# Optimization experiments

Measured on AMD Instinct MI355X. Metric: run time of the kernel, lower is better.

Reference implementation:

```python
import jax, jax.numpy as jnp
import numpy as np

N = 50000      # nodes
E = 800000     # edges
IN = 128       # input feature dim
HID = 64       # out_channels per head
HEADS = 2
OUT = 40       # num classes
SLOPE = 0.2    # leaky relu negative slope
EPS = 1e-16    # PyG softmax denominator epsilon


def _xavier(key, shape):
    fan_out, fan_in = shape[0], shape[1]
    a = float(np.sqrt(6.0 / (fan_in + fan_out)))
    return jax.random.uniform(key, shape, minval=-a, maxval=a, dtype=jnp.float32)


def setup_inputs() -> dict:
    key = jax.random.key(0)
    ks = jax.random.split(key, 16)
    x = jax.random.normal(ks[0], (N, IN), dtype=jnp.float32)
    edge_index = jax.random.randint(ks[1], (2, E), 0, N, dtype=jnp.int64)
    # GAT layer 1: lin_l == lin_r (shared), weight [H*C, in], att [C, H]
    W1 = _xavier(ks[2], (HEADS * HID, IN))
    b1 = jnp.zeros((HEADS * HID,), jnp.float32)
    al1 = _xavier(ks[3], (HID, HEADS))
    ar1 = _xavier(ks[4], (HID, HEADS))
    # GAT layer 2: input dim = heads*hidden
    W2 = _xavier(ks[5], (HEADS * HID, HEADS * HID))
    b2 = jnp.zeros((HEADS * HID,), jnp.float32)
    al2 = _xavier(ks[6], (HID, HEADS))
    ar2 = _xavier(ks[7], (HID, HEADS))
    # post_mp: Linear(heads*hid, hid) -> Linear(hid, out)
    Wp1 = _xavier(ks[8], (HID, HEADS * HID))
    bp1 = jnp.zeros((HID,), jnp.float32)
    Wp2 = _xavier(ks[9], (OUT, HID))
    bp2 = jnp.zeros((OUT,), jnp.float32)
    return dict(x=x, edge_index=edge_index, W1=W1, b1=b1, al1=al1, ar1=ar1,
                W2=W2, b2=b2, al2=al2, ar2=ar2, Wp1=Wp1, bp1=bp1, Wp2=Wp2, bp2=bp2)


def gat_layer(x, edge_index, W, b, att_l, att_r):
    """One GAT layer: shared linear, per-edge leaky-relu scores,
    segment-softmax keyed by destination node, scatter-sum."""
    n = x.shape[0]
    xt = (x @ W.T + b).reshape(n, HEADS, HID)          # [N, H, C] (x_l == x_r)
    alpha_l = jnp.einsum('nhc,ch->nh', xt, att_l)      # [N, H]
    alpha_r = jnp.einsum('nhc,ch->nh', xt, att_r)      # [N, H]
    src, dst = edge_index[0], edge_index[1]            # j = source, i = dest
    e = jax.nn.leaky_relu(alpha_r[dst] + alpha_l[src], SLOPE)   # [E, H]
    # segment softmax over edges grouped by destination node
    seg_max = jax.ops.segment_max(e, dst, num_segments=n)       # [N, H]
    ex = jnp.exp(e - seg_max[dst])
    denom = jax.ops.segment_sum(ex, dst, num_segments=n)        # [N, H]
    alpha = ex / (denom[dst] + EPS)                              # [E, H]
    msg = alpha[:, :, None] * xt[src]                            # [E, H, C]
    out = jax.ops.segment_sum(msg, dst, num_segments=n)          # [N, H, C]
    return out.reshape(n, HEADS * HID)


def reference(x, edge_index, W1, b1, al1, ar1, W2, b2, al2, ar2, Wp1, bp1, Wp2, bp2):
    h = jax.nn.relu(gat_layer(x, edge_index, W1, b1, al1, ar1))
    h = jax.nn.relu(gat_layer(h, edge_index, W2, b2, al2, ar2))
    h = h @ Wp1.T + bp1
    h = h @ Wp2.T + bp2
    return jax.nn.log_softmax(h, axis=1)
```

## Files before the change

kernel.cpp:

```cpp
#include <hip/hip_runtime.h>
#include <hip/hip_fp16.h>
#include <cmath>

#define N_NODES 50000
#define N_EDGES 800000
#define F 128
#define OUT_DIM 40
#define SLOPE 0.2f
#define EPS_DEN 1e-16f

#define BK_SHIFT 7
#define BKSZ 128
#define NBK ((N_NODES + BKSZ - 1) / BKSZ)
#define BK_CAP2 2560
#define SC_CHUNK 2500
#define SC_BLOCKS ((N_EDGES + SC_CHUNK - 1) / SC_CHUNK)
#define GEMM_TILES ((N_NODES + 127) / 128)
#define A_BLOCKS (SC_BLOCKS + 25 + GEMM_TILES)
#define SMEM_BYTES 21504
#define POISON ((int)0xAAAAAAAA)

typedef _Float16 half8 __attribute__((ext_vector_type(8)));
typedef float floatx4 __attribute__((ext_vector_type(4)));

struct ScatterS { int sd[SC_CHUNK]; short sb[SC_CHUNK]; int h[NBK]; int lofs[NBK]; };
struct GemmS    { __half Ah[128][40]; __half Bh[128][40]; };
static_assert(sizeof(ScatterS) <= SMEM_BYTES, "scatter LDS");
static_assert(sizeof(GemmS)    <= SMEM_BYTES, "gemm LDS");

__device__ inline float4 load4(const float* p) { return *(const float4*)p; }
__device__ inline float4 load4(const __half* p) {
  uint2 u = *(const uint2*)p;
  float2 a = __half22float2(*(__half2*)&u.x);
  float2 b = __half22float2(*(__half2*)&u.y);
  return make_float4(a.x, a.y, b.x, b.y);
}

__device__ __forceinline__ void scatter_phase(const int* __restrict__ ei,
    int* __restrict__ bcur, int* __restrict__ pairs, int it, int tid, char* smem_) {
  ScatterS* S = (ScatterS*)smem_;
  for (int i = tid; i < NBK; i += 256) S->h[i] = 0;
  __syncthreads();
  int base = it * SC_CHUNK;
  int end = base + SC_CHUNK; if (end > N_EDGES) end = N_EDGES;
  int cnt = end - base;
  for (int e = base + tid; e < end; e += 256) {
    int s = ei[e];
    int d = ei[N_EDGES + e];
    int b = d >> BK_SHIFT;
    S->sd[e - base] = (s << BK_SHIFT) | (d & (BKSZ - 1));
    S->sb[e - base] = (short)b;
    atomicAdd(&S->h[b], 1);
  }
  __syncthreads();
  for (int i = tid; i < NBK; i += 256)
    if (S->h[i]) {
      S->lofs[i] = i * BK_CAP2 + (atomicAdd(&bcur[i], S->h[i]) - POISON);
      S->h[i] = 0;
    }
  __syncthreads();
  for (int i = tid; i < cnt; i += 256) {
    int b = S->sb[i];
    int pos = S->lofs[b] + atomicAdd(&S->h[b], 1);
    pairs[pos] = S->sd[i];
  }
}

__device__ __forceinline__ void combine_phase(const float* __restrict__ Wp1,
    const float* __restrict__ bp1, const float* __restrict__ Wp2,
    const float* __restrict__ bp2, __half* __restrict__ Wch,
    float* __restrict__ bc, int it, int tid) {
  if (it < 24) {
    int idx = it * 256 + tid;
    int o = idx >> 7, k = idx & 127;
    float s = 0.f;
    if (o < OUT_DIM) {
#pragma unroll 8
      for (int j = 0; j < 64; ++j) s += Wp2[o * 64 + j] * Wp1[j * 128 + k];
    }
    Wch[o * 128 + k] = __float2half(s);
  } else if (tid < 48) {
    int o = tid;
    if (o < OUT_DIM) {
      float s = bp2[o];
      for (int j = 0; j < 64; ++j) s += Wp2[o * 64 + j] * bp1[j];
      bc[o] = s;
    } else {
      bc[o] = -1e30f;
    }
  }
}

template <typename T>
__device__ __forceinline__ void gemm_phase(const T* __restrict__ A,
    const float* __restrict__ W, const float* __restrict__ b,
    const float* __restrict__ attl, const float* __restrict__ attr,
    __half* __restrict__ Ch, float* __restrict__ al, float* __restrict__ ar,
    int nrows, int tile, int tid, char* smem_) {
  GemmS* S = (GemmS*)smem_;
  int lane = tid & 63, wid = tid >> 6;
  int quad = lane >> 4, col = lane & 15;
  int r0 = tile * 128;
  int rowhalf = wid >> 1, colhalf = wid & 1;
  floatx4 acc[4][4] = {};
  for (int kc = 0; kc < 128; kc += 32) {
    for (int i = tid; i < 512; i += 256) {
      int row = i >> 2, seg = i & 3;
      int gr = r0 + row;
      float4 v0, v1;
      if (gr < nrows) {
        const T* p = A + (size_t)gr * 128 + kc + seg * 8;
        v0 = load4(p); v1 = load4(p + 4);
      } else { v0 = make_float4(0.f,0.f,0.f,0.f); v1 = v0; }
      __half2 h0 = __floats2half2_rn(v0.x, v0.y), h1 = __floats2half2_rn(v0.z, v0.w);
      __half2 h2 = __floats2half2_rn(v1.x, v1.y), h3 = __floats2half2_rn(v1.z, v1.w);
      uint4 pk; pk.x = *(unsigned*)&h0; pk.y = *(unsigned*)&h1;
      pk.z = *(unsigned*)&h2; pk.w = *(unsigned*)&h3;
      *(uint4*)&S->Ah[row][seg * 8] = pk;
      const float* q = W + (size_t)row * 128 + kc + seg * 8;
      float4 w0 = *(const float4*)q, w1 = *(const float4*)(q + 4);
      __half2 g0 = __floats2half2_rn(w0.x, w0.y), g1 = __floats2half2_rn(w0.z, w0.w);
      __half2 g2 = __floats2half2_rn(w1.x, w1.y), g3 = __floats2half2_rn(w1.z, w1.w);
      uint4 qk; qk.x = *(unsigned*)&g0; qk.y = *(unsigned*)&g1;
      qk.z = *(unsigned*)&g2; qk.w = *(unsigned*)&g3;
      *(uint4*)&S->Bh[row][seg * 8] = qk;
    }
    __syncthreads();
    half8 afr[4], bfr[4];
#pragma unroll
    for (int rt = 0; rt < 4; ++rt)
      afr[rt] = *(const half8*)&S->Ah[rowhalf * 64 + rt * 16 + col][quad * 8];
#pragma unroll
    for (int ct = 0; ct < 4; ++ct)
      bfr[ct] = *(const half8*)&S->Bh[colhalf * 64 + ct * 16 + col][quad * 8];
#pragma unroll
    for (int rt = 0; rt < 4; ++rt)
#pragma unroll
      for (int ct = 0; ct < 4; ++ct)
        acc[rt][ct] = __builtin_amdgcn_mfma_f32_16x16x32_f16(afr[rt], bfr[ct],
                                                             acc[rt][ct], 0, 0, 0);
    __syncthreads();
  }
  int head = colhalf;
  float bj[4], wl4[4], wr4[4];
#pragma unroll
  for (int ct = 0; ct < 4; ++ct) {
    int c = ct * 16 + col;
    bj[ct] = b[head * 64 + c];
    wl4[ct] = attl[c * 2 + head];
    wr4[ct] = attr[c * 2 + head];
  }
#pragma unroll
  for (int rt = 0; rt < 4; ++rt) {
#pragma unroll
    for (int reg = 0; reg < 4; ++reg) {
      int gr = r0 + rowhalf * 64 + rt * 16 + quad * 4 + reg;
      bool ok = gr < nrows;
      float pl = 0.f, pr = 0.f;
#pragma unroll
      for (int ct = 0; ct < 4; ++ct) {
        float v = acc[rt][ct][reg] + bj[ct];
        pl += v * wl4[ct]; pr += v * wr4[ct];
        if (ok) Ch[(size_t)gr * F + head * 64 + ct * 16 + col] = __float2half(v);
      }
      pl += __shfl_xor(pl, 1, 64); pr += __shfl_xor(pr, 1, 64);
      pl += __shfl_xor(pl, 2, 64); pr += __shfl_xor(pr, 2, 64);
      pl += __shfl_xor(pl, 4, 64); pr += __shfl_xor(pr, 4, 64);
      pl += __shfl_xor(pl, 8, 64); pr += __shfl_xor(pr, 8, 64);
      if (ok && col == 0) { al[gr * 2 + head] = pl; ar[gr * 2 + head] = pr; }
    }
  }
}

__global__ __launch_bounds__(256) void kernelA(const int* __restrict__ ei,
    int* __restrict__ bcur, int* __restrict__ pairs,
    const float* __restrict__ Wp1, const float* __restrict__ bp1,
    const float* __restrict__ Wp2, const float* __restrict__ bp2,
    __half* __restrict__ Wch, float* __restrict__ bc,
    const float* __restrict__ x, const float* __restrict__ W1,
    const float* __restrict__ b1, const float* __restrict__ al1,
    const float* __restrict__ ar1, __half* __restrict__ xh,
    float* __restrict__ al, float* __restrict__ ar) {
  __shared__ __align__(16) char smem[SMEM_BYTES];
  int bid = blockIdx.x, tid = threadIdx.x;
  if (bid < SC_BLOCKS) {
    scatter_phase(ei, bcur, pairs, bid, tid, smem);
  } else if (bid < SC_BLOCKS + 25) {
    combine_phase(Wp1, bp1, Wp2, bp2, Wch, bc, bid - SC_BLOCKS, tid);
  } else {
    gemm_phase<float>(x, W1, b1, al1, ar1, xh, al, ar, N_NODES,
                      bid - SC_BLOCKS - 25, tid, smem);
  }
}

__global__ __launch_bounds__(256) void gemm2_kernel(const __half* __restrict__ hb,
    const float* __restrict__ W2, const float* __restrict__ b2,
    const float* __restrict__ al2, const float* __restrict__ ar2,
    __half* __restrict__ xh, float* __restrict__ al, float* __restrict__ ar) {
  __shared__ __align__(16) char smem[SMEM_BYTES];
  gemm_phase<__half>(hb, W2, b2, al2, ar2, xh, al, ar, N_NODES,
                     blockIdx.x, threadIdx.x, smem);
}

__global__ __launch_bounds__(256) void local_sort(const int* __restrict__ bcur,
    const int* __restrict__ pairs, int* __restrict__ rowstart,
    int* __restrict__ rowend, int* __restrict__ srcs) {
  __shared__ int buf[BK_CAP2];
  __shared__ int sorted[BK_CAP2];
  __shared__ int hist[BKSZ];
  __shared__ int cur[BKSZ];
  int tid = threadIdx.x;
  int b = blockIdx.x;
  int base = b * BK_CAP2;
  int cnt = bcur[b] - POISON;
  if (cnt > BK_CAP2) cnt = BK_CAP2;
  if (cnt < 0) cnt = 0;
  if (tid < BKSZ) hist[tid] = 0;
  __syncthreads();
  for (int i = tid; i < cnt; i += 256) {
    int p = pairs[base + i];
    buf[i] = p;
    atomicAdd(&hist[p & (BKSZ - 1)], 1);
  }
  __syncthreads();
  if (tid < 64) {
    int lane = tid;
    int carry = 0;
#pragma unroll
    for (int c = 0; c < BKSZ; c += 64) {
      int v = hist[c + lane];
      int x = v;
#pragma unroll
      for (int off = 1; off < 64; off <<= 1) {
        int t = __shfl_up(x, off, 64);
        if (lane >= off) x += t;
      }
      int excl = carry + x - v;
      cur[c + lane] = excl;
      int node = b * BKSZ + c + lane;
      if (node < N_NODES) {
        rowstart[node] = base + excl;
        rowend[node]   = base + excl + v;
      }
      carry += __shfl(x, 63, 64);
    }
  }
  __syncthreads();
  for (int i = tid; i < cnt; i += 256) {
    int p = buf[i];
    int pos = atomicAdd(&cur[p & (BKSZ - 1)], 1);
    sorted[pos] = p >> BK_SHIFT;
  }
  __syncthreads();
  for (int i = tid; i < cnt; i += 256)
    srcs[base + i] = sorted[i];
}

__global__ __launch_bounds__(256) void aggregate_kernel(const int* __restrict__ rowstart,
    const int* __restrict__ rowend, const int* __restrict__ srcs,
    const float* __restrict__ al, const float* __restrict__ ar,
    const __half* __restrict__ xh, __half* __restrict__ out, int n) {
  __shared__ float ebuf[4][2][64];
  __shared__ int   sbuf[4][64];
  int tid = threadIdx.x;
  int wid = tid >> 6, lane = tid & 63;
  int g = lane >> 4, q = lane & 15;
  int head = q >> 3;
  int node = blockIdx.x * 4 + wid;
  if (node >= n) return;
  int start = rowstart[node], end = rowend[node];
  float2 arv = *(const float2*)(ar + (size_t)node * 2);
  float ar0 = arv.x, ar1 = arv.y;
  const float* wrow = &ebuf[wid][head][0];
  const __half* xbase = xh + q * 8;
  float acc[8] = {};
  float dl0 = 0.f, dl1 = 0.f;
  for (int c = start; c < end; c += 64) {
    int j = c + lane;
    float e0 = 0.f, e1 = 0.f; int soff = 0;
    if (j < end) {
      int s = srcs[j];
      soff = s << BK_SHIFT;
      float2 a = *(const float2*)(al + (size_t)s * 2);
      float s0 = a.x + ar0; s0 = (s0 > 0.f) ? s0 : SLOPE * s0;
      float s1 = a.y + ar1; s1 = (s1 > 0.f) ? s1 : SLOPE * s1;
      e0 = __expf(s0); e1 = __expf(s1);
    }
    dl0 += e0; dl1 += e1;
    ebuf[wid][0][lane] = e0; ebuf[wid][1][lane] = e1; sbuf[wid][lane] = soff;
    __builtin_amdgcn_wave_barrier();
    int cend = end - c; if (cend > 64) cend = 64;
#pragma unroll 4
    for (int t = 0; t < cend; t += 4) {
      int te = t + g;
      if (te < cend) {
        int so = sbuf[wid][te];
        float w = wrow[te];
        uint4 u = *(const uint4*)(xbase + so);
        const __half2* hh = (const __half2*)&u;
        float2 f0 = __half22float2(hh[0]);
        float2 f1 = __half22float2(hh[1]);
        float2 f2 = __half22float2(hh[2]);
        float2 f3 = __half22float2(hh[3]);
        acc[0] += w * f0.x; acc[1] += w * f0.y;
        acc[2] += w * f1.x; acc[3] += w * f1.y;
        acc[4] += w * f2.x; acc[5] += w * f2.y;
        acc[6] += w * f3.x; acc[7] += w * f3.y;
      }
    }
    __builtin_amdgcn_wave_barrier();
  }
#pragma unroll
  for (int off = 32; off > 0; off >>= 1) {
    dl0 += __shfl_xor(dl0, off, 64);
    dl1 += __shfl_xor(dl1, off, 64);
  }
#pragma unroll
  for (int k = 0; k < 8; ++k) {
    acc[k] += __shfl_xor(acc[k], 16, 64);
    acc[k] += __shfl_xor(acc[k], 32, 64);
  }
  if (g == 0) {
    float d = (head == 0) ? dl0 : dl1;
    float inv = 1.f / (d + EPS_DEN);
    __half2 o0 = __floats2half2_rn(fmaxf(acc[0] * inv, 0.f), fmaxf(acc[1] * inv, 0.f));
    __half2 o1 = __floats2half2_rn(fmaxf(acc[2] * inv, 0.f), fmaxf(acc[3] * inv, 0.f));
    __half2 o2 = __floats2half2_rn(fmaxf(acc[4] * inv, 0.f), fmaxf(acc[5] * inv, 0.f));
    __half2 o3 = __floats2half2_rn(fmaxf(acc[6] * inv, 0.f), fmaxf(acc[7] * inv, 0.f));
    uint4 pack;
    pack.x = *(unsigned*)&o0; pack.y = *(unsigned*)&o1;
    pack.z = *(unsigned*)&o2; pack.w = *(unsigned*)&o3;
    *(uint4*)(out + (size_t)node * F + q * 8) = pack;
  }
}

__global__ __launch_bounds__(256) void post_mfma(const __half* __restrict__ hb,
    const __half* __restrict__ Wch, const float* __restrict__ bc,
    float* __restrict__ out, int n) {
  int tid = threadIdx.x;
  int lane = tid & 63, wid = tid >> 6;
  int quad = lane >> 4, col = lane & 15;
  int base = blockIdx.x * 64 + wid * 16;
  int arow = base + col;
  int asafe = (arow < n) ? arow : (n - 1);
  floatx4 acc[3] = {};
#pragma unroll
  for (int kc = 0; kc < 128; kc += 32) {
    half8 afr = *(const half8*)(hb + (size_t)asafe * F + kc + quad * 8);
#pragma unroll
    for (int ct = 0; ct < 3; ++ct) {
      half8 bfr = *(const half8*)(Wch + (size_t)(ct * 16 + col) * 128 + kc + quad * 8);
      acc[ct] = __builtin_amdgcn_mfma_f32_16x16x32_f16(afr, bfr, acc[ct], 0, 0, 0);
    }
  }
  float bcv[3];
#pragma unroll
  for (int ct = 0; ct < 3; ++ct) bcv[ct] = bc[ct * 16 + col];
#pragma unroll
  for (int reg = 0; reg < 4; ++reg) {
    int row = base + quad * 4 + reg;
    float z[3], m = -INFINITY;
#pragma unroll
    for (int ct = 0; ct < 3; ++ct) { z[ct] = acc[ct][reg] + bcv[ct]; m = fmaxf(m, z[ct]); }
    m = fmaxf(m, __shfl_xor(m, 1, 64));
    m = fmaxf(m, __shfl_xor(m, 2, 64));
    m = fmaxf(m, __shfl_xor(m, 4, 64));
    m = fmaxf(m, __shfl_xor(m, 8, 64));
    float s = 0.f;
#pragma unroll
    for (int ct = 0; ct < 3; ++ct) s += __expf(z[ct] - m);
    s += __shfl_xor(s, 1, 64);
    s += __shfl_xor(s, 2, 64);
    s += __shfl_xor(s, 4, 64);
    s += __shfl_xor(s, 8, 64);
    float ls = logf(s);
    if (row < n) {
#pragma unroll
      for (int ct = 0; ct < 3; ++ct) {
        int o = ct * 16 + col;
        if (o < OUT_DIM) out[(size_t)row * OUT_DIM + o] = z[ct] - m - ls;
      }
    }
  }
}

extern "C" void kernel_launch(void* const* d_in, const int* in_sizes, int n_in,
                              void* d_out, int out_size, void* d_ws, size_t ws_size,
                              hipStream_t stream) {
  const float* x   = (const float*)d_in[0];
  const int*   ei  = (const int*)d_in[1];
  const float* W1  = (const float*)d_in[2];
  const float* b1  = (const float*)d_in[3];
  const float* al1 = (const float*)d_in[4];
  const float* ar1 = (const float*)d_in[5];
  const float* W2  = (const float*)d_in[6];
  const float* b2  = (const float*)d_in[7];
  const float* al2 = (const float*)d_in[8];
  const float* ar2 = (const float*)d_in[9];
  const float* Wp1 = (const float*)d_in[10];
  const float* bp1 = (const float*)d_in[11];
  const float* Wp2 = (const float*)d_in[12];
  const float* bp2 = (const float*)d_in[13];
  float* out = (float*)d_out;

  float* al    = (float*)d_ws;
  float* ar    = al + (size_t)N_NODES * 2;
  __half* Wch  = (__half*)(ar + (size_t)N_NODES * 2);
  float* bc    = (float*)(Wch + 48 * 128);
  int* rowstart= (int*)(bc + 48);
  int* rowend  = rowstart + N_NODES;
  int* bcur    = rowend + N_NODES;
  int* srcs    = bcur + NBK;
  int* pairs   = srcs + NBK * BK_CAP2;
  uintptr_t pp = ((uintptr_t)(pairs + NBK * BK_CAP2) + 255) & ~(uintptr_t)255;
  __half* xh   = (__half*)pp;
  __half* hb   = xh + (size_t)N_NODES * F;

  int nwgrid = (N_NODES + 3) / 4;

  kernelA<<<A_BLOCKS, 256, 0, stream>>>(ei, bcur, pairs, Wp1, bp1, Wp2, bp2,
                                        Wch, bc, x, W1, b1, al1, ar1, xh, al, ar);
  local_sort<<<NBK, 256, 0, stream>>>(bcur, pairs, rowstart, rowend, srcs);
  aggregate_kernel<<<nwgrid, 256, 0, stream>>>(rowstart, rowend, srcs, al, ar, xh, hb, N_NODES);
  gemm2_kernel<<<GEMM_TILES, 256, 0, stream>>>(hb, W2, b2, al2, ar2, xh, al, ar);
  aggregate_kernel<<<nwgrid, 256, 0, stream>>>(rowstart, rowend, srcs, al, ar, xh, hb, N_NODES);
  post_mfma<<<(N_NODES + 63) / 64, 256, 0, stream>>>(hb, Wch, bc, out, N_NODES);
}
```

Baseline: 218.0 us.

## Fuse GAT aggregation with following GEMM via LDS tiles in 1024-thread blocks

```diff
diff --git a/kernel.cpp b/kernel.cpp
--- a/kernel.cpp
+++ b/kernel.cpp
@@ -27,6 +27,10 @@
 struct GemmS    { __half Ah[128][40]; __half Bh[128][40]; };
 static_assert(sizeof(ScatterS) <= SMEM_BYTES, "scatter LDS");
 static_assert(sizeof(GemmS)    <= SMEM_BYTES, "gemm LDS");
+
+__device__ __forceinline__ int swz(int row, int chunk) {
+  return row * 128 + ((chunk ^ (row & 15)) << 3);
+}
 
 __device__ inline float4 load4(const float* p) { return *(const float4*)p; }
 __device__ inline float4 load4(const __half* p) {
@@ -91,6 +95,7 @@
   }
 }
 
+__global__ void local_sort_fwd();
 template <typename T>
 __device__ __forceinline__ void gemm_phase(const T* __restrict__ A,
     const float* __restrict__ W, const float* __restrict__ b,
@@ -193,15 +198,6 @@
   }
 }
 
-__global__ __launch_bounds__(256) void gemm2_kernel(const __half* __restrict__ hb,
-    const float* __restrict__ W2, const float* __restrict__ b2,
-    const float* __restrict__ al2, const float* __restrict__ ar2,
-    __half* __restrict__ xh, float* __restrict__ al, float* __restrict__ ar) {
-  __shared__ __align__(16) char smem[SMEM_BYTES];
-  gemm_phase<__half>(hb, W2, b2, al2, ar2, xh, al, ar, N_NODES,
-                     blockIdx.x, threadIdx.x, smem);
-}
-
 __global__ __launch_bounds__(256) void local_sort(const int* __restrict__ bcur,
     const int* __restrict__ pairs, int* __restrict__ rowstart,
     int* __restrict__ rowend, int* __restrict__ srcs) {
@@ -256,23 +252,26 @@
     srcs[base + i] = sorted[i];
 }
 
-__global__ __launch_bounds__(256) void aggregate_kernel(const int* __restrict__ rowstart,
+__device__ __forceinline__ void agg_node_to_lds(const int* __restrict__ rowstart,
     const int* __restrict__ rowend, const int* __restrict__ srcs,
     const float* __restrict__ al, const float* __restrict__ ar,
-    const __half* __restrict__ xh, __half* __restrict__ out, int n) {
-  __shared__ float ebuf[4][2][64];
-  __shared__ int   sbuf[4][64];
-  int tid = threadIdx.x;
-  int wid = tid >> 6, lane = tid & 63;
+    const __half* __restrict__ xsrc, __half* __restrict__ ldsA,
+    float (*ebufw)[64], int* sbufw, int node, int ldsrow, int lane) {
   int g = lane >> 4, q = lane & 15;
   int head = q >> 3;
-  int node = blockIdx.x * 4 + wid;
-  if (node >= n) return;
+  if (node >= N_NODES) {
+    if (g == 0) {
+      uint4 z = {0, 0, 0, 0};
+      *(uint4*)&ldsA[swz(ldsrow, q)] = z;
+    }
+    __builtin_amdgcn_wave_barrier();
+    return;
+  }
   int start = rowstart[node], end = rowend[node];
   float2 arv = *(const float2*)(ar + (size_t)node * 2);
   float ar0 = arv.x, ar1 = arv.y;
-  const float* wrow = &ebuf[wid][head][0];
-  const __half* xbase = xh + q * 8;
+  const float* wrow = &ebufw[head][0];
+  const __half* xbase = xsrc + q * 8;
   float acc[8] = {};
   float dl0 = 0.f, dl1 = 0.f;
   for (int c = start; c < end; c += 64) {
@@ -287,14 +286,14 @@
       e0 = __expf(s0); e1 = __expf(s1);
     }
     dl0 += e0; dl1 += e1;
-    ebuf[wid][0][lane] = e0; ebuf[wid][1][lane] = e1; sbuf[wid][lane] = soff;
+    ebufw[0][lane] = e0; ebufw[1][lane] = e1; sbufw[lane] = soff;
     __builtin_amdgcn_wave_barrier();
     int cend = end - c; if (cend > 64) cend = 64;
 #pragma unroll 4
     for (int t = 0; t < cend; t += 4) {
       int te = t + g;
       if (te < cend) {
-        int so = sbuf[wid][te];
+        int so = sbufw[te];
         float w = wrow[te];
         uint4 u = *(const uint4*)(xbase + so);
         const __half2* hh = (const __half2*)&u;
@@ -330,26 +329,115 @@
     uint4 pack;
     pack.x = *(unsigned*)&o0; pack.y = *(unsigned*)&o1;
     pack.z = *(unsigned*)&o2; pack.w = *(unsigned*)&o3;
-    *(uint4*)(out + (size_t)node * F + q * 8) = pack;
-  }
-}
-
-__global__ __launch_bounds__(256) void post_mfma(const __half* __restrict__ hb,
+    *(uint4*)&ldsA[swz(ldsrow, q)] = pack;
+  }
+  __builtin_amdgcn_wave_barrier();
+}
+
+__global__ __launch_bounds__(1024) void fusedB(const int* __restrict__ rowstart,
+    const int* __restrict__ rowend, const int* __restrict__ srcs,
+    const float* __restrict__ al, const float* __restrict__ ar,
+    const __half* __restrict__ xh,
+    const float* __restrict__ W2, const float* __restrict__ b2,
+    const float* __restrict__ attl, const float* __restrict__ attr,
+    __half* __restrict__ xh2, float* __restrict__ al2, float* __restrict__ ar2) {
+  __shared__ __half Ah[128 * 128];
+  __shared__ __half Bh[128 * 128];
+  __shared__ float ebuf[16][2][64];
+  __shared__ int   sbuf[16][64];
+  int tid = threadIdx.x;
+  int wid = tid >> 6, lane = tid & 63;
+  int tile = blockIdx.x;
+#pragma unroll
+  for (int r = 0; r < 2; ++r) {
+    int j = tid + r * 1024;
+    int row = j >> 4, c = j & 15;
+    const float* q = W2 + (size_t)row * 128 + c * 8;
+    float4 w0 = *(const float4*)q, w1 = *(const float4*)(q + 4);
+    __half2 g0 = __floats2half2_rn(w0.x, w0.y), g1 = __floats2half2_rn(w0.z, w0.w);
+    __half2 g2 = __floats2half2_rn(w1.x, w1.y), g3 = __floats2half2_rn(w1.z, w1.w);
+    uint4 qk; qk.x = *(unsigned*)&g0; qk.y = *(unsigned*)&g1;
+    qk.z = *(unsigned*)&g2; qk.w = *(unsigned*)&g3;
+    *(uint4*)&Bh[swz(row, c)] = qk;
+  }
+#pragma unroll 1
+  for (int r = 0; r < 8; ++r) {
+    int ldsrow = r * 16 + wid;
+    agg_node_to_lds(rowstart, rowend, srcs, al, ar, xh, Ah,
+                    ebuf[wid], sbuf[wid], tile * 128 + ldsrow, ldsrow, lane);
+  }
+  __syncthreads();
+  int rowg = wid >> 1, colg = wid & 1;
+  int quad = lane >> 4, col = lane & 15;
+  floatx4 acc[4] = {};
+#pragma unroll
+  for (int kc4 = 0; kc4 < 4; ++kc4) {
+    int arow = rowg * 16 + col;
+    half8 afr = *(const half8*)&Ah[swz(arow, (kc4 << 2) | quad)];
+#pragma unroll
+    for (int ct = 0; ct < 4; ++ct) {
+      int brow = colg * 64 + ct * 16 + col;
+      half8 bfr = *(const half8*)&Bh[swz(brow, (kc4 << 2) | quad)];
+      acc[ct] = __builtin_amdgcn_mfma_f32_16x16x32_f16(afr, bfr, acc[ct], 0, 0, 0);
+    }
+  }
+  int head = colg;
+  float bj[4], wl4[4], wr4[4];
+#pragma unroll
+  for (int ct = 0; ct < 4; ++ct) {
+    int c = ct * 16 + col;
+    bj[ct] = b2[head * 64 + c];
+    wl4[ct] = attl[c * 2 + head];
+    wr4[ct] = attr[c * 2 + head];
+  }
+#pragma unroll
+  for (int reg = 0; reg < 4; ++reg) {
+    int gr = tile * 128 + rowg * 16 + quad * 4 + reg;
+    bool ok = gr < N_NODES;
+    float pl = 0.f, pr = 0.f;
+#pragma unroll
+    for (int ct = 0; ct < 4; ++ct) {
+      float v = acc[ct][reg] + bj[ct];
+      pl += v * wl4[ct]; pr += v * wr4[ct];
+      if (ok) xh2[(size_t)gr * F + head * 64 + ct * 16 + col] = __float2half(v);
+    }
+    pl += __shfl_xor(pl, 1, 64); pr += __shfl_xor(pr, 1, 64);
+    pl += __shfl_xor(pl, 2, 64); pr += __shfl_xor(pr, 2, 64);
+    pl += __shfl_xor(pl, 4, 64); pr += __shfl_xor(pr, 4, 64);
+    pl += __shfl_xor(pl, 8, 64); pr += __shfl_xor(pr, 8, 64);
+    if (ok && col == 0) { al2[gr * 2 + head] = pl; ar2[gr * 2 + head] = pr; }
+  }
+}
+
+__global__ __launch_bounds__(1024) void fusedC(const int* __restrict__ rowstart,
+    const int* __restrict__ rowend, const int* __restrict__ srcs,
+    const float* __restrict__ al2, const float* __restrict__ ar2,
+    const __half* __restrict__ xh2,
     const __half* __restrict__ Wch, const float* __restrict__ bc,
-    float* __restrict__ out, int n) {
+    float* __restrict__ out) {
+  __shared__ __half Ah[128 * 128];
+  __shared__ float ebuf[16][2][64];
+  __shared__ int   sbuf[16][64];
   int tid = threadIdx.x;
-  int lane = tid & 63, wid = tid >> 6;
+  int wid = tid >> 6, lane = tid & 63;
+  int tile = blockIdx.x;
+#pragma unroll 1
+  for (int r = 0; r < 8; ++r) {
+    int ldsrow = r * 16 + wid;
+    agg_node_to_lds(rowstart, rowend, srcs, al2, ar2, xh2, Ah,
+                    ebuf[wid], sbuf[wid], tile * 128 + ldsrow, ldsrow, lane);
+  }
+  __syncthreads();
+  if (wid >= 8) return;
   int quad = lane >> 4, col = lane & 15;
-  int base = blockIdx.x * 64 + wid * 16;
-  int arow = base + col;
-  int asafe = (arow < n) ? arow : (n - 1);
+  int rbase = wid * 16;
   floatx4 acc[3] = {};
 #pragma unroll
-  for (int kc = 0; kc < 128; kc += 32) {
-    half8 afr = *(const half8*)(hb + (size_t)asafe * F + kc + quad * 8);
+  for (int kc4 = 0; kc4 < 4; ++kc4) {
+    half8 afr = *(const half8*)&Ah[swz(rbase + col, (kc4 << 2) | quad)];
 #pragma unroll
     for (int ct = 0; ct < 3; ++ct) {
-      half8 bfr = *(const half8*)(Wch + (size_t)(ct * 16 + col) * 128 + kc + quad * 8);
+      half8 bfr = *(const half8*)(Wch + (size_t)(ct * 16 + col) * 128 + kc4 * 32 + quad * 8);
       acc[ct] = __builtin_amdgcn_mfma_f32_16x16x32_f16(afr, bfr, acc[ct], 0, 0, 0);
     }
   }
@@ -358,7 +446,7 @@
   for (int ct = 0; ct < 3; ++ct) bcv[ct] = bc[ct * 16 + col];
 #pragma unroll
   for (int reg = 0; reg < 4; ++reg) {
-    int row = base + quad * 4 + reg;
+    int row = tile * 128 + rbase + quad * 4 + reg;
     float z[3], m = -INFINITY;
 #pragma unroll
     for (int ct = 0; ct < 3; ++ct) { z[ct] = acc[ct][reg] + bcv[ct]; m = fmaxf(m, z[ct]); }
@@ -374,7 +462,7 @@
     s += __shfl_xor(s, 4, 64);
     s += __shfl_xor(s, 8, 64);
     float ls = logf(s);
-    if (row < n) {
+    if (row < N_NODES) {
 #pragma unroll
       for (int ct = 0; ct < 3; ++ct) {
         int o = ct * 16 + col;
@@ -395,8 +483,8 @@
   const float* ar1 = (const float*)d_in[5];
   const float* W2  = (const float*)d_in[6];
   const float* b2  = (const float*)d_in[7];
-  const float* al2 = (const float*)d_in[8];
-  const float* ar2 = (const float*)d_in[9];
+  const float* al2w= (const float*)d_in[8];
+  const float* ar2w= (const float*)d_in[9];
   const float* Wp1 = (const float*)d_in[10];
   const float* bp1 = (const float*)d_in[11];
   const float* Wp2 = (const float*)d_in[12];
@@ -405,7 +493,9 @@
 
   float* al    = (float*)d_ws;
   float* ar    = al + (size_t)N_NODES * 2;
-  __half* Wch  = (__half*)(ar + (size_t)N_NODES * 2);
+  float* al2   = ar + (size_t)N_NODES * 2;
+  float* ar2   = al2 + (size_t)N_NODES * 2;
+  __half* Wch  = (__half*)(ar2 + (size_t)N_NODES * 2);
   float* bc    = (float*)(Wch + 48 * 128);
   int* rowstart= (int*)(bc + 48);
   int* rowend  = rowstart + N_NODES;
@@ -414,15 +504,13 @@
   int* pairs   = srcs + NBK * BK_CAP2;
   uintptr_t pp = ((uintptr_t)(pairs + NBK * BK_CAP2) + 255) & ~(uintptr_t)255;
   __half* xh   = (__half*)pp;
-  __half* hb   = xh + (size_t)N_NODES * F;
-
-  int nwgrid = (N_NODES + 3) / 4;
+  __half* xh2  = xh + (size_t)N_NODES * F;
 
   kernelA<<<A_BLOCKS, 256, 0, stream>>>(ei, bcur, pairs, Wp1, bp1, Wp2, bp2,
                                         Wch, bc, x, W1, b1, al1, ar1, xh, al, ar);
   local_sort<<<NBK, 256, 0, stream>>>(bcur, pairs, rowstart, rowend, srcs);
-  aggregate_kernel<<<nwgrid, 256, 0, stream>>>(rowstart, rowend, srcs, al, ar, xh, hb, N_NODES);
-  gemm2_kernel<<<GEMM_TILES, 256, 0, stream>>>(hb, W2, b2, al2, ar2, xh, al, ar);
-  aggregate_kernel<<<nwgrid, 256, 0, stream>>>(rowstart, rowend, srcs, al, ar, xh, hb, N_NODES);
-  post_mfma<<<(N_NODES + 63) / 64, 256, 0, stream>>>(hb, Wch, bc, out, N_NODES);
-}
+  fusedB<<<GEMM_TILES, 1024, 0, stream>>>(rowstart, rowend, srcs, al, ar, xh,
+                                          W2, b2, al2w, ar2w, xh2, al2, ar2);
+  fusedC<<<GEMM_TILES, 1024, 0, stream>>>(rowstart, rowend, srcs, al2, ar2, xh2,
+                                          Wch, bc, out);
+}
```

New measurement: 215.9 us. Within noise of the previous version (-1.0%).
